# Kernel optimization log

Hardware: AMD Instinct MI355X
Metric: run time of the kernel (lower is better)

The kernel has to match this reference:

```python
import jax, jax.numpy as jnp
import numpy as np

B, NI, LS, D, H, W, LAB = 512, 256, 64, 8, 128, 256, 10
L = LS - 1          # logsig_dim - 1 (leading term dropped)
NSTEPS = 256        # fixed Tsit5 steps over [t0, t1]

# Tsit5 Butcher tableau (Tsitouras 2011)
C2, C3, C4, C5, C6 = 0.161, 0.327, 0.9, 0.9800255409045097, 1.0
A21 = 0.161
A31, A32 = -0.008480655492356989, 0.335480655492357
A41, A42, A43 = 2.8971530571054935, -6.359448489975075, 4.3622954328695815
A51, A52, A53, A54 = 5.325864828439257, -11.748883564062828, 7.4955393428898365, -0.09249506636175525
A61, A62, A63, A64, A65 = 5.86145544294642, -12.92096931784711, 8.159367898576159, -0.071584973281401, -0.028269050394068383
B1, B2, B3, B4, B5, B6 = 0.09646076681806523, 0.01, 0.4798896504144996, 1.379008574103742, -3.290069515436081, 2.324710524099774


def setup_inputs() -> dict:
    key = jax.random.key(0)
    ks = jax.random.split(key, 8)

    def lin(k, out_d, in_d):  # eqx.nn.Linear default init: U(-1/sqrt(in), 1/sqrt(in))
        kw, kb = jax.random.split(k)
        lim = 1.0 / np.sqrt(in_d)
        Wm = jax.random.uniform(kw, (out_d, in_d), minval=-lim, maxval=lim, dtype=jnp.float32)
        bv = jax.random.uniform(kb, (out_d,), minval=-lim, maxval=lim, dtype=jnp.float32)
        return Wm, bv

    W0, b0 = lin(ks[0], W, H)        # VF MLP layer 1
    W1, b1 = lin(ks[1], W, W)        # VF MLP layer 2
    W2, b2 = lin(ks[2], H * L, W)    # VF MLP output layer
    l1w, l1b = lin(ks[3], H, D)      # linear1
    l2w, l2b = lin(ks[4], LAB, H)    # linear2

    ts = jnp.linspace(0.0, 1.0, NI + 1, dtype=jnp.float32)
    intervals = ts[1:]               # right endpoints for searchsorted lookup
    logsig = 0.1 * jax.random.normal(ks[5], (B, NI, LS), dtype=jnp.float32)
    x0 = jax.random.normal(ks[6], (B, D), dtype=jnp.float32)
    return dict(ts=ts, intervals=intervals, logsig=logsig, x0=x0,
                W0=W0, b0=b0, W1=W1, b1=b1, W2=W2, b2=b2,
                l1w=l1w, l1b=l1b, l2w=l2w, l2b=l2b)


def _forward(ts, intervals, logsig, x0, W0, b0, W1, b1, W2, b2, l1w, l1b, l2w, l2b):
    def f(t, y):  # y: [B, H] -> dy/dt: [B, H]
        idx = jnp.clip(jnp.searchsorted(intervals, t), 0, NI - 1)
        h = jax.nn.silu(y @ W0.T + b0)
        h = jax.nn.silu(h @ W1.T + b1)
        A = jnp.tanh(h @ W2.T + b2).reshape(-1, H, L)   # [B, H, L]
        g = logsig[:, idx, 1:]                           # [B, L]
        return jnp.einsum('bhl,bl->bh', A, g)

    y0 = x0 @ l1w.T + l1b                                # linear1
    dt = (ts[-1] - ts[0]) / NSTEPS

    @jax.checkpoint
    def step(carry, _):
        t, y = carry
        k1 = f(t, y)
        k2 = f(t + C2 * dt, y + dt * (A21 * k1))
        k3 = f(t + C3 * dt, y + dt * (A31 * k1 + A32 * k2))
        k4 = f(t + C4 * dt, y + dt * (A41 * k1 + A42 * k2 + A43 * k3))
        k5 = f(t + C5 * dt, y + dt * (A51 * k1 + A52 * k2 + A53 * k3 + A54 * k4))
        k6 = f(t + C6 * dt, y + dt * (A61 * k1 + A62 * k2 + A63 * k3 + A64 * k4 + A65 * k5))
        y_new = y + dt * (B1 * k1 + B2 * k2 + B3 * k3 + B4 * k4 + B5 * k5 + B6 * k6)
        return (t + dt, y_new), None

    (_, yf), _ = jax.lax.scan(step, (ts[0], y0), None, length=NSTEPS)
    return jax.nn.softmax(yf @ l2w.T + l2b, axis=-1)     # classification head


def reference(ts, intervals, logsig, x0, W0, b0, W1, b1, W2, b2, l1w, l1b, l2w, l2b):
    return _forward(ts, intervals, logsig, x0, W0, b0, W1, b1, W2, b2, l1w, l1b, l2w, l2b)
```

## Files before the change

### kernel.cpp

```cpp
#include <hip/hip_runtime.h>

typedef __attribute__((ext_vector_type(8))) short short8;
typedef __attribute__((ext_vector_type(4))) float f32x4;
typedef unsigned long long ull;

#define DT (1.0f/256.0f)
#define NSTEPS 256

__device__ __forceinline__ short f2bf(float f) {
    unsigned u = __float_as_uint(f);
    u = (u + 0x7fffu + ((u >> 16) & 1u)) >> 16;
    return (short)u;
}
__device__ __forceinline__ unsigned cvtpk(float a, float b) {
    unsigned r;
    asm("v_cvt_pk_bf16_f32 %0, %1, %2" : "=v"(r) : "v"(a), "v"(b));
    return r;
}
__device__ __forceinline__ float fast_silu(float x) {
    float e = __expf(-x);
    return x * __builtin_amdgcn_rcpf(1.f + e);
}
__device__ __forceinline__ float fast_tanh(float x) {
    float e = __expf(2.f * x);
    return 1.f - 2.f * __builtin_amdgcn_rcpf(e + 1.f);
}

__device__ __forceinline__ void st_agent_f(float* p, float v) {
    __hip_atomic_store(p, v, __ATOMIC_RELAXED, __HIP_MEMORY_SCOPE_AGENT);
}
__device__ __forceinline__ void st_agent_u32(unsigned* p, unsigned v) {
    __hip_atomic_store(p, v, __ATOMIC_RELAXED, __HIP_MEMORY_SCOPE_AGENT);
}
__device__ __forceinline__ ull ld_agent_u64(const void* p) {
    return __hip_atomic_load((const ull*)p, __ATOMIC_RELAXED, __HIP_MEMORY_SCOPE_AGENT);
}

__global__ void perm_w0(const float* __restrict__ W0, short* __restrict__ W0p) {
    int i = blockIdx.x * 256 + threadIdx.x;
    int j = i & 7, l = (i >> 3) & 63, kc = (i >> 9) & 3, ot = i >> 11;
    int row = ot * 16 + (l & 15);
    int col = kc * 32 + ((l >> 4) << 3) + j;
    W0p[i] = f2bf(W0[row * 128 + col]);
}
__global__ void perm_w1(const float* __restrict__ W1, short* __restrict__ W1p) {
    int i = blockIdx.x * 256 + threadIdx.x;
    int j = i & 7, l = (i >> 3) & 63, kc = (i >> 9) & 7, ot = i >> 12;
    int row = ot * 16 + (l & 15);
    int col = kc * 32 + ((l >> 4) << 3) + j;
    W1p[i] = f2bf(W1[row * 256 + col]);
}
__global__ void perm_w2(const float* __restrict__ W2, short* __restrict__ W2p) {
    int i = blockIdx.x * 256 + threadIdx.x;
    int j = i & 7, ln = (i >> 3) & 63, kc = (i >> 9) & 7;
    int q4 = (i >> 12) & 15, ht = i >> 16;
    int m = ln & 15;
    int hl = m & 3, lvin = m >> 2;
    int lv = q4 * 4 + lvin;
    if (lv >= 63) { W2p[i] = 0; return; }
    int row = (ht * 4 + hl) * 63 + lv;
    int col = kc * 32 + ((ln >> 4) << 3) + j;
    W2p[i] = f2bf(W2[row * 256 + col]);
}

__global__ void y0_kernel(const float* __restrict__ x0, const float* __restrict__ l1w,
                          const float* __restrict__ l1b, float* __restrict__ y0f,
                          unsigned short* __restrict__ ybf) {
    int i = blockIdx.x * 256 + threadIdx.x;
    int b = i >> 7, h = i & 127;
    float s = l1b[h];
    #pragma unroll
    for (int d = 0; d < 8; ++d) s += x0[b * 8 + d] * l1w[h * 8 + d];
    y0f[i] = s;
    ybf[i] = (unsigned short)f2bf(s);
}

struct Smem {
    alignas(16) short ysb[32 * 136];
    alignas(16) short h1b[32 * 272];
    alignas(16) short h2b[32 * 272];
    float gshA[32 * 65];
    float gshB[32 * 65];
    float b2sh[4 * 64];
    float b0sh[256];
    float b1sh[256];
    float kred[8][2][4][17];
};

__constant__ const float cA2[1] = {0.161f};
__constant__ const float cA3[2] = {-0.008480655492356989f, 0.335480655492357f};
__constant__ const float cA4[3] = {2.8971530571054935f, -6.359448489975075f, 4.3622954328695815f};
__constant__ const float cA5[4] = {5.325864828439257f, -11.748883564062828f, 7.4955393428898365f, -0.09249506636175525f};
__constant__ const float cA6[5] = {5.86145544294642f, -12.92096931784711f, 8.159367898576159f, -0.071584973281401f, -0.028269050394068383f};

template<int STAGE>
__device__ __forceinline__ void do_stage(
    Smem& sm, float* __restrict__ gsh, int s, int gsi, int bg, int ht, int tid,
    unsigned short* __restrict__ ybf,
    float* __restrict__ yfinal,
    const short* __restrict__ W0p, const short* __restrict__ W1p, const short* __restrict__ W2p,
    const float* __restrict__ logsig,
    unsigned* __restrict__ barctr,
    float (&yreg)[2], float (&kr)[2][5])
{
    const int w    = tid >> 6;
    const int lane = tid & 63;
    const int q    = lane >> 4;
    const int rr   = lane & 15;
    const unsigned short* ycur = ybf + (gsi & 1) * 65536;
    unsigned short*       ynxt = ybf + ((gsi + 1) & 1) * 65536;

    short8 af0[2][4];
    #pragma unroll
    for (int oi = 0; oi < 2; ++oi)
        #pragma unroll
        for (int kc = 0; kc < 4; ++kc)
            af0[oi][kc] = *reinterpret_cast<const short8*>(W0p + ((w * 2 + oi) * 4 + kc) * 512 + lane * 8);

    if constexpr (STAGE == 2) {
        const int b = tid >> 4, l0 = (tid & 15) * 4;
        const float* gp = logsig + (bg * 32 + b) * 16384 + s * 64 + 1;
        #pragma unroll
        for (int ii = 0; ii < 4; ++ii) {
            int l = l0 + ii;
            gsh[b * 65 + l] = (l < 63) ? gp[l] : 0.f;
        }
    }

    if (gsi > 0 && tid == 0) {
        const unsigned target = 32u * (unsigned)gsi;
        while (__hip_atomic_load(&barctr[bg * 16], __ATOMIC_RELAXED, __HIP_MEMORY_SCOPE_AGENT) < target) { }
    }
    __syncthreads();

    {
        const int b = tid >> 4, h0 = (tid & 15) * 8;
        const ull* src = (const ull*)(ycur + (bg * 32 + b) * 128 + h0);
        ull v0 = ld_agent_u64(src + 0);
        ull v1 = ld_agent_u64(src + 1);
        ull* dst = (ull*)&sm.ysb[b * 136 + h0];
        dst[0] = v0; dst[1] = v1;
    }
    __syncthreads();

    {
        f32x4 acc[2][2];
        #pragma unroll
        for (int oi = 0; oi < 2; ++oi)
            #pragma unroll
            for (int bq = 0; bq < 2; ++bq) acc[oi][bq] = (f32x4){0.f, 0.f, 0.f, 0.f};
        #pragma unroll
        for (int kc = 0; kc < 4; ++kc) {
            short8 bfr[2];
            #pragma unroll
            for (int bq = 0; bq < 2; ++bq)
                bfr[bq] = *reinterpret_cast<const short8*>(&sm.ysb[(bq * 16 + rr) * 136 + kc * 32 + q * 8]);
            #pragma unroll
            for (int oi = 0; oi < 2; ++oi)
                #pragma unroll
                for (int bq = 0; bq < 2; ++bq)
                    acc[oi][bq] = __builtin_amdgcn_mfma_f32_16x16x32_bf16(af0[oi][kc], bfr[bq], acc[oi][bq], 0, 0, 0);
        }
        #pragma unroll
        for (int oi = 0; oi < 2; ++oi) {
            const int ho = (w * 2 + oi) * 16 + q * 4;
            #pragma unroll
            for (int bq = 0; bq < 2; ++bq) {
                float vv[4];
                #pragma unroll
                for (int j = 0; j < 4; ++j)
                    vv[j] = fast_silu(acc[oi][bq][j] + sm.b0sh[ho + j]);
                ull pk = (ull)cvtpk(vv[0], vv[1]) | ((ull)cvtpk(vv[2], vv[3]) << 32);
                *reinterpret_cast<ull*>(&sm.h1b[(bq * 16 + rr) * 272 + ho]) = pk;
            }
        }
    }
    __syncthreads();

    {
        short8 af[2][8];
        #pragma unroll
        for (int oi = 0; oi < 2; ++oi)
            #pragma unroll
            for (int kc = 0; kc < 8; ++kc)
                af[oi][kc] = *reinterpret_cast<const short8*>(W1p + ((w * 2 + oi) * 8 + kc) * 512 + lane * 8);
        f32x4 acc[2][2];
        #pragma unroll
        for (int oi = 0; oi < 2; ++oi)
            #pragma unroll
            for (int bq = 0; bq < 2; ++bq) acc[oi][bq] = (f32x4){0.f, 0.f, 0.f, 0.f};
        #pragma unroll
        for (int kc = 0; kc < 8; ++kc) {
            short8 bfr[2];
            #pragma unroll
            for (int bq = 0; bq < 2; ++bq)
                bfr[bq] = *reinterpret_cast<const short8*>(&sm.h1b[(bq * 16 + rr) * 272 + kc * 32 + q * 8]);
            #pragma unroll
            for (int oi = 0; oi < 2; ++oi)
                #pragma unroll
                for (int bq = 0; bq < 2; ++bq)
                    acc[oi][bq] = __builtin_amdgcn_mfma_f32_16x16x32_bf16(af[oi][kc], bfr[bq], acc[oi][bq], 0, 0, 0);
        }
        #pragma unroll
        for (int oi = 0; oi < 2; ++oi) {
            const int ho = (w * 2 + oi) * 16 + q * 4;
            #pragma unroll
            for (int bq = 0; bq < 2; ++bq) {
                float vv[4];
                #pragma unroll
                for (int j = 0; j < 4; ++j)
                    vv[j] = fast_silu(acc[oi][bq][j] + sm.b1sh[ho + j]);
                ull pk = (ull)cvtpk(vv[0], vv[1]) | ((ull)cvtpk(vv[2], vv[3]) << 32);
                *reinterpret_cast<ull*>(&sm.h2b[(bq * 16 + rr) * 272 + ho]) = pk;
            }
        }
    }
    __syncthreads();

    {
        short8 af[2][8];
        #pragma unroll
        for (int t2 = 0; t2 < 2; ++t2)
            #pragma unroll
            for (int kc = 0; kc < 8; ++kc)
                af[t2][kc] = *reinterpret_cast<const short8*>(W2p + (size_t)(ht * 16 + w * 2 + t2) * 4096 + kc * 512 + lane * 8);
        f32x4 acc[2][2];
        #pragma unroll
        for (int t2 = 0; t2 < 2; ++t2)
            #pragma unroll
            for (int bq = 0; bq < 2; ++bq) acc[t2][bq] = (f32x4){0.f, 0.f, 0.f, 0.f};
        #pragma unroll
        for (int kc = 0; kc < 8; ++kc) {
            short8 bfr[2];
            #pragma unroll
            for (int bq = 0; bq < 2; ++bq)
                bfr[bq] = *reinterpret_cast<const short8*>(&sm.h2b[(bq * 16 + rr) * 272 + kc * 32 + q * 8]);
            #pragma unroll
            for (int t2 = 0; t2 < 2; ++t2)
                #pragma unroll
                for (int bq = 0; bq < 2; ++bq)
                    acc[t2][bq] = __builtin_amdgcn_mfma_f32_16x16x32_bf16(af[t2][kc], bfr[bq], acc[t2][bq], 0, 0, 0);
        }
        float kacc[2][4];
        #pragma unroll
        for (int bq = 0; bq < 2; ++bq)
            #pragma unroll
            for (int j = 0; j < 4; ++j) kacc[bq][j] = 0.f;
        #pragma unroll
        for (int t2 = 0; t2 < 2; ++t2) {
            const int lv = (w * 2 + t2) * 4 + q;
            #pragma unroll
            for (int bq = 0; bq < 2; ++bq) {
                float gv = gsh[(bq * 16 + rr) * 65 + lv];
                #pragma unroll
                for (int j = 0; j < 4; ++j) {
                    float x = acc[t2][bq][j] + sm.b2sh[j * 64 + lv];
                    kacc[bq][j] += fast_tanh(x) * gv;
                }
            }
        }
        #pragma unroll
        for (int bq = 0; bq < 2; ++bq)
            #pragma unroll
            for (int j = 0; j < 4; ++j) {
                float v = kacc[bq][j];
                v += __shfl_xor(v, 16);
                v += __shfl_xor(v, 32);
                kacc[bq][j] = v;
            }
        if (q == 0) {
            #pragma unroll
            for (int bq = 0; bq < 2; ++bq)
                #pragma unroll
                for (int j = 0; j < 4; ++j)
                    sm.kred[w][bq][j][rr] = kacc[bq][j];
        }
    }
    __syncthreads();

    if (tid < 64) {
        const int b = tid >> 1, hs = tid & 1;
        float s0 = 0.f, s1 = 0.f;
        #pragma unroll
        for (int ww = 0; ww < 8; ++ww) {
            s0 += sm.kred[ww][b >> 4][hs * 2 + 0][b & 15];
            s1 += sm.kred[ww][b >> 4][hs * 2 + 1][b & 15];
        }
        float nv0, nv1;
        if constexpr (STAGE == 1) {
            kr[0][0] = s0; kr[1][0] = s1;
            nv0 = yreg[0] + DT * (cA2[0] * s0);
            nv1 = yreg[1] + DT * (cA2[0] * s1);
        } else if constexpr (STAGE == 2) {
            kr[0][1] = s0; kr[1][1] = s1;
            nv0 = yreg[0] + DT * (cA3[0] * kr[0][0] + cA3[1] * s0);
            nv1 = yreg[1] + DT * (cA3[0] * kr[1][0] + cA3[1] * s1);
        } else if constexpr (STAGE == 3) {
            kr[0][2] = s0; kr[1][2] = s1;
            nv0 = yreg[0] + DT * (cA4[0] * kr[0][0] + cA4[1] * kr[0][1] + cA4[2] * s0);
            nv1 = yreg[1] + DT * (cA4[0] * kr[1][0] + cA4[1] * kr[1][1] + cA4[2] * s1);
        } else if constexpr (STAGE == 4) {
            kr[0][3] = s0; kr[1][3] = s1;
            nv0 = yreg[0] + DT * (cA5[0] * kr[0][0] + cA5[1] * kr[0][1] + cA5[2] * kr[0][2] + cA5[3] * s0);
            nv1 = yreg[1] + DT * (cA5[0] * kr[1][0] + cA5[1] * kr[1][1] + cA5[2] * kr[1][2] + cA5[3] * s1);
        } else if constexpr (STAGE == 5) {
            kr[0][4] = s0; kr[1][4] = s1;
            nv0 = yreg[0] + DT * (cA6[0] * kr[0][0] + cA6[1] * kr[0][1] + cA6[2] * kr[0][2] + cA6[3] * kr[0][3] + cA6[4] * s0);
            nv1 = yreg[1] + DT * (cA6[0] * kr[1][0] + cA6[1] * kr[1][1] + cA6[2] * kr[1][2] + cA6[3] * kr[1][3] + cA6[4] * s1);
        } else {
            nv0 = yreg[0] + DT * (0.09646076681806523f * kr[0][0] + 0.01f * kr[0][1]
                 + 0.4798896504144996f * kr[0][2] + 1.379008574103742f * kr[0][3]
                 + (-3.290069515436081f) * kr[0][4] + 2.324710524099774f * s0);
            nv1 = yreg[1] + DT * (0.09646076681806523f * kr[1][0] + 0.01f * kr[1][1]
                 + 0.4798896504144996f * kr[1][2] + 1.379008574103742f * kr[1][3]
                 + (-3.290069515436081f) * kr[1][4] + 2.324710524099774f * s1);
            yreg[0] = nv0; yreg[1] = nv1;
        }
        const int gi = (bg * 32 + b) * 128 + ht * 4 + hs * 2;
        st_agent_u32(reinterpret_cast<unsigned*>(ynxt + gi), cvtpk(nv0, nv1));
        if constexpr (STAGE == 6) {
            if (s == NSTEPS - 1) {
                st_agent_f(&yfinal[gi], nv0);
                st_agent_f(&yfinal[gi + 1], nv1);
            }
        }
    }

    __syncthreads();
    if (tid == 0)
        __hip_atomic_fetch_add(&barctr[bg * 16], 1u, __ATOMIC_RELAXED, __HIP_MEMORY_SCOPE_AGENT);
}

__global__ __launch_bounds__(512, 2) void rde_persistent(
    float* y0f, unsigned short* ybf, float* yfinal, unsigned* barctr,
    const short* W0p, const short* W1p, const short* W2p,
    const float* b0, const float* b1, const float* b2,
    const float* logsig)
{
    __shared__ Smem sm;
    const int tid = threadIdx.x;
    const int pr  = blockIdx.x >> 5;
    const int ht  = blockIdx.x & 31;
    const int bgA = pr * 2;
    const int bgB = pr * 2 + 1;
    if (tid < 256) {
        sm.b0sh[tid] = b0[tid];
        int hl = tid >> 6, lv = tid & 63;
        sm.b2sh[tid] = (lv < 63) ? b2[(ht * 4 + hl) * 63 + lv] : 0.f;
    } else {
        sm.b1sh[tid - 256] = b1[tid - 256];
    }
    {
        const int b = tid >> 4, l0 = (tid & 15) * 4;
        const float* gpA = logsig + (bgA * 32 + b) * 16384 + 1;
        const float* gpB = logsig + (bgB * 32 + b) * 16384 + 1;
        #pragma unroll
        for (int ii = 0; ii < 4; ++ii) {
            int l = l0 + ii;
            sm.gshA[b * 65 + l] = (l < 63) ? gpA[l] : 0.f;
            sm.gshB[b * 65 + l] = (l < 63) ? gpB[l] : 0.f;
        }
    }
    float yrA[2] = {0.f, 0.f}, yrB[2] = {0.f, 0.f};
    float krA[2][5] = {{0.f,0.f,0.f,0.f,0.f},{0.f,0.f,0.f,0.f,0.f}};
    float krB[2][5] = {{0.f,0.f,0.f,0.f,0.f},{0.f,0.f,0.f,0.f,0.f}};
    if (tid < 64) {
        const int b = tid >> 1, hs = tid & 1;
        const int giA = (bgA * 32 + b) * 128 + ht * 4 + hs * 2;
        const int giB = (bgB * 32 + b) * 128 + ht * 4 + hs * 2;
        yrA[0] = y0f[giA]; yrA[1] = y0f[giA + 1];
        yrB[0] = y0f[giB]; yrB[1] = y0f[giB + 1];
    }
    #pragma unroll 1
    for (int s = 0; s < NSTEPS; ++s) {
        const int g6 = s * 6;
        do_stage<1>(sm, sm.gshA, s, g6 + 0, bgA, ht, tid, ybf, yfinal, W0p, W1p, W2p, logsig, barctr, yrA, krA);
        do_stage<1>(sm, sm.gshB, s, g6 + 0, bgB, ht, tid, ybf, yfinal, W0p, W1p, W2p, logsig, barctr, yrB, krB);
        do_stage<2>(sm, sm.gshA, s, g6 + 1, bgA, ht, tid, ybf, yfinal, W0p, W1p, W2p, logsig, barctr, yrA, krA);
        do_stage<2>(sm, sm.gshB, s, g6 + 1, bgB, ht, tid, ybf, yfinal, W0p, W1p, W2p, logsig, barctr, yrB, krB);
        do_stage<3>(sm, sm.gshA, s, g6 + 2, bgA, ht, tid, ybf, yfinal, W0p, W1p, W2p, logsig, barctr, yrA, krA);
        do_stage<3>(sm, sm.gshB, s, g6 + 2, bgB, ht, tid, ybf, yfinal, W0p, W1p, W2p, logsig, barctr, yrB, krB);
        do_stage<4>(sm, sm.gshA, s, g6 + 3, bgA, ht, tid, ybf, yfinal, W0p, W1p, W2p, logsig, barctr, yrA, krA);
        do_stage<4>(sm, sm.gshB, s, g6 + 3, bgB, ht, tid, ybf, yfinal, W0p, W1p, W2p, logsig, barctr, yrB, krB);
        do_stage<5>(sm, sm.gshA, s, g6 + 4, bgA, ht, tid, ybf, yfinal, W0p, W1p, W2p, logsig, barctr, yrA, krA);
        do_stage<5>(sm, sm.gshB, s, g6 + 4, bgB, ht, tid, ybf, yfinal, W0p, W1p, W2p, logsig, barctr, yrB, krB);
        do_stage<6>(sm, sm.gshA, s, g6 + 5, bgA, ht, tid, ybf, yfinal, W0p, W1p, W2p, logsig, barctr, yrA, krA);
        do_stage<6>(sm, sm.gshB, s, g6 + 5, bgB, ht, tid, ybf, yfinal, W0p, W1p, W2p, logsig, barctr, yrB, krB);
    }
}

__global__ void out_kernel(const float* __restrict__ yf, const float* __restrict__ l2w,
                           const float* __restrict__ l2b, float* __restrict__ out) {
    int b = blockIdx.x, t = threadIdx.x;
    float ya = yf[b * 128 + t], yb = yf[b * 128 + 64 + t];
    __shared__ float lg[10];
    for (int c = 0; c < 10; ++c) {
        float p = ya * l2w[c * 128 + t] + yb * l2w[c * 128 + 64 + t];
        for (int off = 32; off > 0; off >>= 1) p += __shfl_down(p, off);
        if (t == 0) lg[c] = p + l2b[c];
    }
    __syncthreads();
    if (t == 0) {
        float m = lg[0];
        for (int c = 1; c < 10; ++c) m = fmaxf(m, lg[c]);
        float s = 0.f, e[10];
        for (int c = 0; c < 10; ++c) { e[c] = expf(lg[c] - m); s += e[c]; }
        for (int c = 0; c < 10; ++c) out[b * 10 + c] = e[c] / s;
    }
}

extern "C" void kernel_launch(void* const* d_in, const int* in_sizes, int n_in,
                              void* d_out, int out_size, void* d_ws, size_t ws_size,
                              hipStream_t stream) {
    const float* logsig = (const float*)d_in[2];
    const float* x0  = (const float*)d_in[3];
    const float* W0  = (const float*)d_in[4];
    const float* b0  = (const float*)d_in[5];
    const float* W1  = (const float*)d_in[6];
    const float* b1  = (const float*)d_in[7];
    const float* W2  = (const float*)d_in[8];
    const float* b2  = (const float*)d_in[9];
    const float* l1w = (const float*)d_in[10];
    const float* l1b = (const float*)d_in[11];
    const float* l2w = (const float*)d_in[12];
    const float* l2b = (const float*)d_in[13];
    float* out = (float*)d_out;

    char* ws = (char*)d_ws;
    float*          y0f    = (float*)(ws);
    unsigned short* ybf    = (unsigned short*)(ws + 262144);
    float*          yfinal = (float*)(ws + 524288);
    short*          W0p    = (short*)(ws + 786432);
    short*          W1p    = (short*)(ws + 851968);
    short*          W2p    = (short*)(ws + 983040);
    unsigned*       barctr = (unsigned*)(ws + 5177344);

    hipMemsetAsync(barctr, 0, 16 * 16 * sizeof(unsigned), stream);
    perm_w0<<<128, 256, 0, stream>>>(W0, W0p);
    perm_w1<<<256, 256, 0, stream>>>(W1, W1p);
    perm_w2<<<8192, 256, 0, stream>>>(W2, W2p);
    y0_kernel<<<256, 256, 0, stream>>>(x0, l1w, l1b, y0f, ybf);

    void* args[] = {&y0f, &ybf, &yfinal, &barctr, &W0p, &W1p, &W2p, &b0, &b1, &b2, &logsig};
    hipLaunchCooperativeKernel((const void*)rde_persistent, dim3(256), dim3(512), args, 0, stream);

    out_kernel<<<512, 64, 0, stream>>>(yfinal, l2w, l2b, out);
}
```

Measured before the change: 18.67 ms.

## Rework block partition: one batch group per block, 8 hidden units each

Each persistent block now owns a single 32-sample batch group and 8 hidden outputs across 16 blocks, instead of two batch groups and 4 hidden outputs across 32 blocks. The W2 permutation, the bias and reduction shared-memory layouts, and the inter-block barrier target are adjusted to match. This halves the number of blocks syncing per batch group and removes the interleaved A/B stage calls. In exchange, each block repeats the W2 GEMM twice per stage and has less interleaving available to hide barrier waits. The layer-1 and layer-2 MLP work is still replicated in every block.

After: 22.90 ms. 22.7% more time.

```diff
diff --git a/kernel.cpp b/kernel.cpp
--- a/kernel.cpp
+++ b/kernel.cpp
@@ -53,12 +53,13 @@
 __global__ void perm_w2(const float* __restrict__ W2, short* __restrict__ W2p) {
     int i = blockIdx.x * 256 + threadIdx.x;
     int j = i & 7, ln = (i >> 3) & 63, kc = (i >> 9) & 7;
-    int q4 = (i >> 12) & 15, ht = i >> 16;
+    int t = (i >> 12) & 31, ht = i >> 17;
+    int h4loc = t >> 4, q4 = t & 15;
     int m = ln & 15;
     int hl = m & 3, lvin = m >> 2;
     int lv = q4 * 4 + lvin;
     if (lv >= 63) { W2p[i] = 0; return; }
-    int row = (ht * 4 + hl) * 63 + lv;
+    int row = (ht * 8 + h4loc * 4 + hl) * 63 + lv;
     int col = kc * 32 + ((ln >> 4) << 3) + j;
     W2p[i] = f2bf(W2[row * 256 + col]);
 }
@@ -79,12 +80,11 @@
     alignas(16) short ysb[32 * 136];
     alignas(16) short h1b[32 * 272];
     alignas(16) short h2b[32 * 272];
-    float gshA[32 * 65];
-    float gshB[32 * 65];
-    float b2sh[4 * 64];
+    float gsh[32 * 65];
+    float b2sh[8 * 64];
     float b0sh[256];
     float b1sh[256];
-    float kred[8][2][4][17];
+    float kred[8][2][8][17];
 };
 
 __constant__ const float cA2[1] = {0.161f};
@@ -95,7 +95,7 @@
 
 template<int STAGE>
 __device__ __forceinline__ void do_stage(
-    Smem& sm, float* __restrict__ gsh, int s, int gsi, int bg, int ht, int tid,
+    Smem& sm, int s, int gsi, int bg, int ht, int tid,
     unsigned short* __restrict__ ybf,
     float* __restrict__ yfinal,
     const short* __restrict__ W0p, const short* __restrict__ W1p, const short* __restrict__ W2p,
@@ -123,12 +123,12 @@
         #pragma unroll
         for (int ii = 0; ii < 4; ++ii) {
             int l = l0 + ii;
-            gsh[b * 65 + l] = (l < 63) ? gp[l] : 0.f;
+            sm.gsh[b * 65 + l] = (l < 63) ? gp[l] : 0.f;
         }
     }
 
     if (gsi > 0 && tid == 0) {
-        const unsigned target = 32u * (unsigned)gsi;
+        const unsigned target = 16u * (unsigned)gsi;
         while (__hip_atomic_load(&barctr[bg * 16], __ATOMIC_RELAXED, __HIP_MEMORY_SCOPE_AGENT) < target) { }
     }
     __syncthreads();
@@ -217,18 +217,23 @@
     }
     __syncthreads();
 
+    float kacc0[2][4], kacc1[2][4];
+    #pragma unroll
+    for (int bq = 0; bq < 2; ++bq)
+        #pragma unroll
+        for (int j = 0; j < 4; ++j) { kacc0[bq][j] = 0.f; kacc1[bq][j] = 0.f; }
     {
         short8 af[2][8];
         #pragma unroll
-        for (int t2 = 0; t2 < 2; ++t2)
+        for (int qq = 0; qq < 2; ++qq)
             #pragma unroll
             for (int kc = 0; kc < 8; ++kc)
-                af[t2][kc] = *reinterpret_cast<const short8*>(W2p + (size_t)(ht * 16 + w * 2 + t2) * 4096 + kc * 512 + lane * 8);
+                af[qq][kc] = *reinterpret_cast<const short8*>(W2p + ((size_t)(ht * 32 + 0 * 16 + w * 2 + qq) * 8 + kc) * 512 + lane * 8);
         f32x4 acc[2][2];
         #pragma unroll
-        for (int t2 = 0; t2 < 2; ++t2)
-            #pragma unroll
-            for (int bq = 0; bq < 2; ++bq) acc[t2][bq] = (f32x4){0.f, 0.f, 0.f, 0.f};
+        for (int qq = 0; qq < 2; ++qq)
+            #pragma unroll
+            for (int bq = 0; bq < 2; ++bq) acc[qq][bq] = (f32x4){0.f, 0.f, 0.f, 0.f};
         #pragma unroll
         for (int kc = 0; kc < 8; ++kc) {
             short8 bfr[2];
@@ -236,55 +241,92 @@
             for (int bq = 0; bq < 2; ++bq)
                 bfr[bq] = *reinterpret_cast<const short8*>(&sm.h2b[(bq * 16 + rr) * 272 + kc * 32 + q * 8]);
             #pragma unroll
-            for (int t2 = 0; t2 < 2; ++t2)
+            for (int qq = 0; qq < 2; ++qq)
                 #pragma unroll
                 for (int bq = 0; bq < 2; ++bq)
-                    acc[t2][bq] = __builtin_amdgcn_mfma_f32_16x16x32_bf16(af[t2][kc], bfr[bq], acc[t2][bq], 0, 0, 0);
-        }
-        float kacc[2][4];
+                    acc[qq][bq] = __builtin_amdgcn_mfma_f32_16x16x32_bf16(af[qq][kc], bfr[bq], acc[qq][bq], 0, 0, 0);
+        }
+        #pragma unroll
+        for (int qq = 0; qq < 2; ++qq) {
+            const int lv = (w * 2 + qq) * 4 + q;
+            #pragma unroll
+            for (int bq = 0; bq < 2; ++bq) {
+                float gv = sm.gsh[(bq * 16 + rr) * 65 + lv];
+                #pragma unroll
+                for (int j = 0; j < 4; ++j) {
+                    float x = acc[qq][bq][j] + sm.b2sh[(0 * 4 + j) * 64 + lv];
+                    kacc0[bq][j] += fast_tanh(x) * gv;
+                }
+            }
+        }
+    }
+    {
+        short8 af[2][8];
+        #pragma unroll
+        for (int qq = 0; qq < 2; ++qq)
+            #pragma unroll
+            for (int kc = 0; kc < 8; ++kc)
+                af[qq][kc] = *reinterpret_cast<const short8*>(W2p + ((size_t)(ht * 32 + 1 * 16 + w * 2 + qq) * 8 + kc) * 512 + lane * 8);
+        f32x4 acc[2][2];
+        #pragma unroll
+        for (int qq = 0; qq < 2; ++qq)
+            #pragma unroll
+            for (int bq = 0; bq < 2; ++bq) acc[qq][bq] = (f32x4){0.f, 0.f, 0.f, 0.f};
+        #pragma unroll
+        for (int kc = 0; kc < 8; ++kc) {
+            short8 bfr[2];
+            #pragma unroll
+            for (int bq = 0; bq < 2; ++bq)
+                bfr[bq] = *reinterpret_cast<const short8*>(&sm.h2b[(bq * 16 + rr) * 272 + kc * 32 + q * 8]);
+            #pragma unroll
+            for (int qq = 0; qq < 2; ++qq)
+                #pragma unroll
+                for (int bq = 0; bq < 2; ++bq)
+                    acc[qq][bq] = __builtin_amdgcn_mfma_f32_16x16x32_bf16(af[qq][kc], bfr[bq], acc[qq][bq], 0, 0, 0);
+        }
+        #pragma unroll
+        for (int qq = 0; qq < 2; ++qq) {
+            const int lv = (w * 2 + qq) * 4 + q;
+            #pragma unroll
+            for (int bq = 0; bq < 2; ++bq) {
+                float gv = sm.gsh[(bq * 16 + rr) * 65 + lv];
+                #pragma unroll
+                for (int j = 0; j < 4; ++j) {
+                    float x = acc[qq][bq][j] + sm.b2sh[(1 * 4 + j) * 64 + lv];
+                    kacc1[bq][j] += fast_tanh(x) * gv;
+                }
+            }
+        }
+    }
+    #pragma unroll
+    for (int bq = 0; bq < 2; ++bq)
+        #pragma unroll
+        for (int j = 0; j < 4; ++j) {
+            float v0 = kacc0[bq][j];
+            v0 += __shfl_xor(v0, 16); v0 += __shfl_xor(v0, 32);
+            kacc0[bq][j] = v0;
+            float v1 = kacc1[bq][j];
+            v1 += __shfl_xor(v1, 16); v1 += __shfl_xor(v1, 32);
+            kacc1[bq][j] = v1;
+        }
+    if (q == 0) {
         #pragma unroll
         for (int bq = 0; bq < 2; ++bq)
             #pragma unroll
-            for (int j = 0; j < 4; ++j) kacc[bq][j] = 0.f;
-        #pragma unroll
-        for (int t2 = 0; t2 < 2; ++t2) {
-            const int lv = (w * 2 + t2) * 4 + q;
-            #pragma unroll
-            for (int bq = 0; bq < 2; ++bq) {
-                float gv = gsh[(bq * 16 + rr) * 65 + lv];
-                #pragma unroll
-                for (int j = 0; j < 4; ++j) {
-                    float x = acc[t2][bq][j] + sm.b2sh[j * 64 + lv];
-                    kacc[bq][j] += fast_tanh(x) * gv;
-                }
-            }
-        }
-        #pragma unroll
-        for (int bq = 0; bq < 2; ++bq)
-            #pragma unroll
             for (int j = 0; j < 4; ++j) {
-                float v = kacc[bq][j];
-                v += __shfl_xor(v, 16);
-                v += __shfl_xor(v, 32);
-                kacc[bq][j] = v;
-            }
-        if (q == 0) {
-            #pragma unroll
-            for (int bq = 0; bq < 2; ++bq)
-                #pragma unroll
-                for (int j = 0; j < 4; ++j)
-                    sm.kred[w][bq][j][rr] = kacc[bq][j];
-        }
-    }
-    __syncthreads();
-
-    if (tid < 64) {
-        const int b = tid >> 1, hs = tid & 1;
+                sm.kred[w][bq][j][rr]     = kacc0[bq][j];
+                sm.kred[w][bq][4 + j][rr] = kacc1[bq][j];
+            }
+    }
+    __syncthreads();
+
+    if (tid < 128) {
+        const int b = tid >> 2, hq = tid & 3;
         float s0 = 0.f, s1 = 0.f;
         #pragma unroll
         for (int ww = 0; ww < 8; ++ww) {
-            s0 += sm.kred[ww][b >> 4][hs * 2 + 0][b & 15];
-            s1 += sm.kred[ww][b >> 4][hs * 2 + 1][b & 15];
+            s0 += sm.kred[ww][b >> 4][hq * 2 + 0][b & 15];
+            s1 += sm.kred[ww][b >> 4][hq * 2 + 1][b & 15];
         }
         float nv0, nv1;
         if constexpr (STAGE == 1) {
@@ -316,7 +358,7 @@
                  + (-3.290069515436081f) * kr[1][4] + 2.324710524099774f * s1);
             yreg[0] = nv0; yreg[1] = nv1;
         }
-        const int gi = (bg * 32 + b) * 128 + ht * 4 + hs * 2;
+        const int gi = (bg * 32 + b) * 128 + ht * 8 + hq * 2;
         st_agent_u32(reinterpret_cast<unsigned*>(ynxt + gi), cvtpk(nv0, nv1));
         if constexpr (STAGE == 6) {
             if (s == NSTEPS - 1) {
@@ -339,53 +381,40 @@
 {
     __shared__ Smem sm;
     const int tid = threadIdx.x;
-    const int pr  = blockIdx.x >> 5;
-    const int ht  = blockIdx.x & 31;
-    const int bgA = pr * 2;
-    const int bgB = pr * 2 + 1;
-    if (tid < 256) {
-        sm.b0sh[tid] = b0[tid];
-        int hl = tid >> 6, lv = tid & 63;
-        sm.b2sh[tid] = (lv < 63) ? b2[(ht * 4 + hl) * 63 + lv] : 0.f;
-    } else {
-        sm.b1sh[tid - 256] = b1[tid - 256];
-    }
+    const int bg  = blockIdx.x >> 4;
+    const int ht  = blockIdx.x & 15;
+    {
+        int hl8 = tid >> 6, lv = tid & 63;
+        sm.b2sh[tid] = (lv < 63) ? b2[(ht * 8 + hl8) * 63 + lv] : 0.f;
+    }
+    if (tid < 256) sm.b0sh[tid] = b0[tid];
+    else           sm.b1sh[tid - 256] = b1[tid - 256];
     {
         const int b = tid >> 4, l0 = (tid & 15) * 4;
-        const float* gpA = logsig + (bgA * 32 + b) * 16384 + 1;
-        const float* gpB = logsig + (bgB * 32 + b) * 16384 + 1;
+        const float* gp = logsig + (bg * 32 + b) * 16384 + 1;
         #pragma unroll
         for (int ii = 0; ii < 4; ++ii) {
             int l = l0 + ii;
-            sm.gshA[b * 65 + l] = (l < 63) ? gpA[l] : 0.f;
-            sm.gshB[b * 65 + l] = (l < 63) ? gpB[l] : 0.f;
-        }
-    }
-    float yrA[2] = {0.f, 0.f}, yrB[2] = {0.f, 0.f};
-    float krA[2][5] = {{0.f,0.f,0.f,0.f,0.f},{0.f,0.f,0.f,0.f,0.f}};
-    float krB[2][5] = {{0.f,0.f,0.f,0.f,0.f},{0.f,0.f,0.f,0.f,0.f}};
-    if (tid < 64) {
-        const int b = tid >> 1, hs = tid & 1;
-        const int giA = (bgA * 32 + b) * 128 + ht * 4 + hs * 2;
-        const int giB = (bgB * 32 + b) * 128 + ht * 4 + hs * 2;
-        yrA[0] = y0f[giA]; yrA[1] = y0f[giA + 1];
-        yrB[0] = y0f[giB]; yrB[1] = y0f[giB + 1];
+            sm.gsh[b * 65 + l] = (l < 63) ? gp[l] : 0.f;
+        }
+    }
+    float yreg[2] = {0.f, 0.f};
+    float kr[2][5] = {{0.f,0.f,0.f,0.f,0.f},{0.f,0.f,0.f,0.f,0.f}};
+    if (tid < 128) {
+        const int b = tid >> 2, hq = tid & 3;
+        const int gi = (bg * 32 + b) * 128 + ht * 8 + hq * 2;
+        yreg[0] = y0f[gi];
+        yreg[1] = y0f[gi + 1];
     }
     #pragma unroll 1
     for (int s = 0; s < NSTEPS; ++s) {
         const int g6 = s * 6;
-        do_stage<1>(sm, sm.gshA, s, g6 + 0, bgA, ht, tid, ybf, yfinal, W0p, W1p, W2p, logsig, barctr, yrA, krA);
-        do_stage<1>(sm, sm.gshB, s, g6 + 0, bgB, ht, tid, ybf, yfinal, W0p, W1p, W2p, logsig, barctr, yrB, krB);
-        do_stage<2>(sm, sm.gshA, s, g6 + 1, bgA, ht, tid, ybf, yfinal, W0p, W1p, W2p, logsig, barctr, yrA, krA);
-        do_stage<2>(sm, sm.gshB, s, g6 + 1, bgB, ht, tid, ybf, yfinal, W0p, W1p, W2p, logsig, barctr, yrB, krB);
-        do_stage<3>(sm, sm.gshA, s, g6 + 2, bgA, ht, tid, ybf, yfinal, W0p, W1p, W2p, logsig, barctr, yrA, krA);
-        do_stage<3>(sm, sm.gshB, s, g6 + 2, bgB, ht, tid, ybf, yfinal, W0p, W1p, W2p, logsig, barctr, yrB, krB);
-        do_stage<4>(sm, sm.gshA, s, g6 + 3, bgA, ht, tid, ybf, yfinal, W0p, W1p, W2p, logsig, barctr, yrA, krA);
-        do_stage<4>(sm, sm.gshB, s, g6 + 3, bgB, ht, tid, ybf, yfinal, W0p, W1p, W2p, logsig, barctr, yrB, krB);
-        do_stage<5>(sm, sm.gshA, s, g6 + 4, bgA, ht, tid, ybf, yfinal, W0p, W1p, W2p, logsig, barctr, yrA, krA);
-        do_stage<5>(sm, sm.gshB, s, g6 + 4, bgB, ht, tid, ybf, yfinal, W0p, W1p, W2p, logsig, barctr, yrB, krB);
-        do_stage<6>(sm, sm.gshA, s, g6 + 5, bgA, ht, tid, ybf, yfinal, W0p, W1p, W2p, logsig, barctr, yrA, krA);
-        do_stage<6>(sm, sm.gshB, s, g6 + 5, bgB, ht, tid, ybf, yfinal, W0p, W1p, W2p, logsig, barctr, yrB, krB);
+        do_stage<1>(sm, s, g6 + 0, bg, ht, tid, ybf, yfinal, W0p, W1p, W2p, logsig, barctr, yreg, kr);
+        do_stage<2>(sm, s, g6 + 1, bg, ht, tid, ybf, yfinal, W0p, W1p, W2p, logsig, barctr, yreg, kr);
+        do_stage<3>(sm, s, g6 + 2, bg, ht, tid, ybf, yfinal, W0p, W1p, W2p, logsig, barctr, yreg, kr);
+        do_stage<4>(sm, s, g6 + 3, bg, ht, tid, ybf, yfinal, W0p, W1p, W2p, logsig, barctr, yreg, kr);
+        do_stage<5>(sm, s, g6 + 4, bg, ht, tid, ybf, yfinal, W0p, W1p, W2p, logsig, barctr, yreg, kr);
+        do_stage<6>(sm, s, g6 + 5, bg, ht, tid, ybf, yfinal, W0p, W1p, W2p, logsig, barctr, yreg, kr);
     }
 }
 
```
